# Optimization experiments

Hardware: AMD Instinct MI355X
Metric: run time of the kernel (lower is better)

The kernel has to match this reference:

```python
import jax, jax.numpy as jnp
import numpy as np

B, N, C, H = 16, 1024, 768, 12
HD = C // H               # head_dim = 64
SCALE = HD ** -0.5
EPS = 1e-5


def ter_quant(w):
    """BitNet-b1.58 ternary weight quantization with straight-through estimator.
    Per-tensor scale = mean(|W|); weights rounded to {-1,0,1}*scale."""
    s = jnp.mean(jnp.abs(w))
    wq = jnp.round(jnp.clip(w / (s + EPS), -1.0, 1.0)) * s
    return w + jax.lax.stop_gradient(wq - w)


def setup_inputs() -> dict:
    key = jax.random.key(0)
    k1, k2, k3 = jax.random.split(key, 3)
    return {
        "x": jax.random.normal(k1, (B, N, C), dtype=jnp.float32),
        "w_qkv": jax.random.normal(k2, (3 * C, C), dtype=jnp.float32) * 0.02,
        "w_proj": jax.random.normal(k3, (C, C), dtype=jnp.float32) * 0.02,
        "b_proj": jnp.zeros((C,), dtype=jnp.float32),
    }


def reference(x, w_qkv, w_proj, b_proj):
    # ternary-quantized QKV projection: [B,N,C] @ [C,3C] -> [B,N,3C]
    qkv = jnp.einsum('bnc,dc->bnd', x, ter_quant(w_qkv))
    qkv = qkv.reshape(B, N, 3, H, HD).transpose(2, 0, 3, 1, 4)  # [3,B,H,N,HD]
    q, k, v = qkv[0], qkv[1], qkv[2]
    # manual softmax attention (dropout p=0 -> identity)
    attn = jax.nn.softmax(jnp.einsum('bhqd,bhkd->bhqk', q, k) * SCALE, axis=-1)
    out = jnp.einsum('bhqk,bhkd->bhqd', attn, v)          # [B,H,N,HD]
    out = out.transpose(0, 2, 1, 3).reshape(B, N, C)      # [B,N,C]
    # ternary-quantized output projection
    return jnp.einsum('bnc,dc->bnd', out, ter_quant(w_proj)) + b_proj
```

## Files before the change

### kernel.cpp

```cpp
#include <hip/hip_runtime.h>
#include <hip/hip_bf16.h>

#define DEVI __device__ __forceinline__

typedef __bf16 bf16_t;
typedef __bf16 bf16x8 __attribute__((ext_vector_type(8)));
typedef float  f32x4  __attribute__((ext_vector_type(4)));
typedef float  f32x16 __attribute__((ext_vector_type(16)));
typedef unsigned short u16x4 __attribute__((ext_vector_type(4)));
typedef unsigned int   u32x4 __attribute__((ext_vector_type(4)));

typedef __attribute__((address_space(1))) unsigned int gas_u32;
typedef __attribute__((address_space(3))) unsigned int las_u32;

#define LOG2E 1.4426950408889634f

DEVI void gload16(const void* g, void* l) {
  __builtin_amdgcn_global_load_lds((gas_u32*)g, (las_u32*)l, 16, 0, 0);
}

DEVI unsigned short bf16bits(float f) {
  bf16_t b = (bf16_t)f;
  return __builtin_bit_cast(unsigned short, b);
}

DEVI unsigned pk2(float a, float b) {
  return ((unsigned)bf16bits(b) << 16) | (unsigned)bf16bits(a);
}

DEVI unsigned short quant1(float wv, double s) {
  double tq = (double)wv / s;
  tq = fmin(fmax(tq, -1.0), 1.0);
  return __builtin_bit_cast(unsigned short, (bf16_t)(float)rint(tq));
}

__global__ __launch_bounds__(256) void k_abssum2(const float* __restrict__ wq,
                                                 const float* __restrict__ wp,
                                                 double* __restrict__ partials) {
  __shared__ double sm[256];
  const int t = threadIdx.x, bid = blockIdx.x;
  const float* __restrict__ w = (bid < 256) ? wq : wp;
  const int n = (bid < 256) ? 1769472 : 589824;
  const int b0 = bid & 255;
  double acc = 0.0;
  for (int i = b0 * 256 + t; i < n; i += 65536)
    acc += (double)fabsf(w[i]);
  sm[t] = acc;
  __syncthreads();
  #pragma unroll
  for (int s = 128; s > 0; s >>= 1) {
    if (t < s) sm[t] += sm[t + s];
    __syncthreads();
  }
  if (t == 0) partials[bid] = sm[0];
}

__global__ __launch_bounds__(256) void k_reduce2(const double* __restrict__ partials,
                                                 double* __restrict__ outs) {
  __shared__ double sm[256];
  const int t = threadIdx.x;
  sm[t] = partials[blockIdx.x * 256 + t];
  __syncthreads();
  #pragma unroll
  for (int s = 128; s > 0; s >>= 1) {
    if (t < s) sm[t] += sm[t + s];
    __syncthreads();
  }
  if (t == 0) outs[blockIdx.x] = sm[0];
}

__global__ __launch_bounds__(256) void k_prep(
    const float* __restrict__ wq, const float* __restrict__ wp,
    const float* __restrict__ x, const double* __restrict__ scl,
    bf16_t* __restrict__ wqs, bf16_t* __restrict__ wps, bf16_t* __restrict__ xbf) {
  const int bid = blockIdx.x, t = threadIdx.x;
  if (bid < 1728) {
    const double s = scl[0] * (1.0 / 1769472.0) + 1e-5;
    const int i = bid * 256 + t;
    const float4 v = ((const float4*)wq)[i];
    u16x4 o = { quant1(v.x, s), quant1(v.y, s), quant1(v.z, s), quant1(v.w, s) };
    ((u16x4*)wqs)[i] = o;
  } else if (bid < 2304) {
    const double s = scl[1] * (1.0 / 589824.0) + 1e-5;
    const int i = (bid - 1728) * 256 + t;
    const float4 v = ((const float4*)wp)[i];
    u16x4 o = { quant1(v.x, s), quant1(v.y, s), quant1(v.z, s), quant1(v.w, s) };
    ((u16x4*)wps)[i] = o;
  } else {
    const int i = (bid - 2304) * 256 + t;
    const float4 v = ((const float4*)x)[i];
    u16x4 pk = { bf16bits(v.x), bf16bits(v.y), bf16bits(v.z), bf16bits(v.w) };
    ((u16x4*)xbf)[i] = pk;
  }
}

template<int MODE>
__global__ __launch_bounds__(512, 2) void k_gemm(
    const bf16_t* __restrict__ A, const bf16_t* __restrict__ Bw,
    const double* __restrict__ sumptr, double invn,
    bf16_t* __restrict__ Qb, bf16_t* __restrict__ Kb, bf16_t* __restrict__ VTb,
    const float* __restrict__ bias, float* __restrict__ Out,
    int nxblk)
{
  __shared__ __align__(16) char lds[147456];
  const int t = threadIdx.x, l = t & 63, w = t >> 6;

  const int nblk = nxblk * 64;
  const int flat = blockIdx.y * nxblk + blockIdx.x;
  const int per = nblk >> 3;
  const int swz = (flat & 7) * per + (flat >> 3);
  const int m0 = (swz / nxblk) * 256, n0 = (swz % nxblk) * 128;

  const int wm = w >> 1, wn = w & 1;
  const int srow = l >> 3, scol = (l & 7) * 8;
  const int lq = l & 15, lh = l >> 4;
  const int gcol = scol ^ (srow * 8);

  auto sA = [&](int slot, int kts, int ha, int c) {
    const int row = ha * 128 + (c * 8 + w) * 8 + srow;
    gload16(A + (size_t)(m0 + row) * 768 + kts * 64 + gcol,
            lds + slot * 49152 + ha * 16384 + (c * 8 + w) * 1024);
  };
  auto sB = [&](int slot, int kts, int c) {
    const int row = (c * 8 + w) * 8 + srow;
    gload16(Bw + (size_t)(n0 + row) * 768 + kts * 64 + gcol,
            lds + slot * 49152 + 32768 + (c * 8 + w) * 1024);
  };

  f32x4 acc[4][4] = {};

  sA(0, 0, 0, 0); sA(0, 0, 0, 1); sA(0, 0, 1, 0); sA(0, 0, 1, 1);
  sB(0, 0, 0);    sB(0, 0, 1);
  sA(1, 1, 0, 0); sA(1, 1, 0, 1); sA(1, 1, 1, 0); sA(1, 1, 1, 1);
  sB(1, 1, 0);    sB(1, 1, 1);
  asm volatile("s_waitcnt vmcnt(6)" ::: "memory");
  asm volatile("s_barrier" ::: "memory");

  #pragma unroll
  for (int kt = 0; kt < 12; ++kt) {
    const char* cA = lds + (kt % 3) * 49152;
    const char* cB = cA + 32768;
    const int st3 = (kt + 2) % 3;
    const bool stg = (kt < 10);

    {
      bf16x8 af[4], bf[4];
      #pragma unroll
      for (int i = 0; i < 4; ++i) {
        const int row = wm * 64 + i * 16 + lq;
        af[i] = *(const bf16x8*)(cA + row * 128 + ((lh * 16) ^ ((row & 7) << 4)));
      }
      #pragma unroll
      for (int j = 0; j < 4; ++j) {
        const int row = wn * 64 + j * 16 + lq;
        bf[j] = *(const bf16x8*)(cB + row * 128 + ((lh * 16) ^ ((row & 7) << 4)));
      }
      if (stg) { sA(st3, kt + 2, 0, 0); sA(st3, kt + 2, 0, 1); sB(st3, kt + 2, 0); }
      asm volatile("s_barrier" ::: "memory");
      __builtin_amdgcn_s_setprio(1);
      #pragma unroll
      for (int i = 0; i < 4; ++i)
        #pragma unroll
        for (int j = 0; j < 4; ++j)
          acc[i][j] = __builtin_amdgcn_mfma_f32_16x16x32_bf16(af[i], bf[j], acc[i][j], 0, 0, 0);
      __builtin_amdgcn_s_setprio(0);
      asm volatile("s_barrier" ::: "memory");
    }
    {
      bf16x8 af[4], bf[4];
      #pragma unroll
      for (int i = 0; i < 4; ++i) {
        const int row = wm * 64 + i * 16 + lq;
        af[i] = *(const bf16x8*)(cA + row * 128 + ((64 + lh * 16) ^ ((row & 7) << 4)));
      }
      #pragma unroll
      for (int j = 0; j < 4; ++j) {
        const int row = wn * 64 + j * 16 + lq;
        bf[j] = *(const bf16x8*)(cB + row * 128 + ((64 + lh * 16) ^ ((row & 7) << 4)));
      }
      if (stg) { sA(st3, kt + 2, 1, 0); sA(st3, kt + 2, 1, 1); sB(st3, kt + 2, 1); }
      asm volatile("s_barrier" ::: "memory");
      __builtin_amdgcn_s_setprio(1);
      #pragma unroll
      for (int i = 0; i < 4; ++i)
        #pragma unroll
        for (int j = 0; j < 4; ++j)
          acc[i][j] = __builtin_amdgcn_mfma_f32_16x16x32_bf16(af[i], bf[j], acc[i][j], 0, 0, 0);
      __builtin_amdgcn_s_setprio(0);
      if (stg) asm volatile("s_waitcnt vmcnt(6)" ::: "memory");
      else     asm volatile("s_waitcnt vmcnt(0)" ::: "memory");
      asm volatile("s_barrier" ::: "memory");
    }
  }

  const float s = (float)((*sumptr) * invn);
  char* st = lds + w * 8192;

  const int mrow0 = m0 + wm * 64;
  const int b = mrow0 >> 10, nbase = mrow0 & 1023;

  if (MODE == 0) {
    const int d0 = n0 + wn * 64;
    const int which = d0 / 768;
    const int hh = (d0 >> 6) % 12;
    if (which == 2) {
      #pragma unroll
      for (int j = 0; j < 4; ++j)
        #pragma unroll
        for (int i = 0; i < 4; ++i)
          #pragma unroll
          for (int r = 0; r < 4; ++r) {
            const int rowd = j * 16 + lq;
            const int coln = (i * 16 + lh * 4 + r) * 2;
            *(bf16_t*)(st + rowd * 128 + (coln ^ ((rowd & 7) << 4))) =
                (bf16_t)(acc[i][j][r] * s);
          }
    } else {
      const float sc = (which == 0) ? s * 0.125f * LOG2E : s;
      #pragma unroll
      for (int i = 0; i < 4; ++i)
        #pragma unroll
        for (int j = 0; j < 4; ++j)
          #pragma unroll
          for (int r = 0; r < 4; ++r) {
            const int row = i * 16 + lh * 4 + r;
            const int colb = (j * 16 + lq) * 2;
            *(bf16_t*)(st + row * 128 + (colb ^ ((row & 7) << 4))) =
                (bf16_t)(acc[i][j][r] * sc);
          }
    }
    __syncthreads();
    if (which == 0) {
      char* dstp = (char*)(Qb + ((size_t)(b * 12 + hh) * 1024 + nbase) * 64);
      #pragma unroll
      for (int it = 0; it < 8; ++it) {
        const int row = it * 8 + (l >> 3);
        const int colb = (l & 7) * 16;
        const u32x4 v = *(const u32x4*)(st + row * 128 + (colb ^ ((row & 7) << 4)));
        *(u32x4*)(dstp + row * 128 + colb) = v;
      }
    } else {
      bf16_t* base = (which == 1) ? Kb : VTb;
      char* dstp = (char*)base + ((((size_t)(b * 12 + hh)) * 16 + (nbase >> 6)) << 13);
      #pragma unroll
      for (int j = 0; j < 8; ++j) {
        const int row = (j >> 2) * 32 + (l & 31);
        const int colb = (j & 3) * 32 + (l >> 5) * 16;
        const u32x4 v = *(const u32x4*)(st + row * 128 + (colb ^ ((row & 7) << 4)));
        *(u32x4*)(dstp + j * 1024 + l * 16) = v;
      }
    }
  } else {
    const int d0 = n0 + wn * 64;
    const float4 bv = *(const float4*)(bias + d0 + (l & 15) * 4);
    #pragma unroll
    for (int c = 0; c < 2; ++c) {
      #pragma unroll
      for (int i2 = 0; i2 < 2; ++i2) {
        const int i = c * 2 + i2;
        #pragma unroll
        for (int j = 0; j < 4; ++j)
          #pragma unroll
          for (int r = 0; r < 4; ++r) {
            const int row = i2 * 16 + lh * 4 + r;
            const int colb = (j * 16 + lq) * 4;
            *(float*)(st + row * 256 + (colb ^ ((row & 7) << 4))) = acc[i][j][r] * s;
          }
      }
      __syncthreads();
      #pragma unroll
      for (int it = 0; it < 8; ++it) {
        const int row = it * 4 + (l >> 4);
        const int colb = (l & 15) * 16;
        float4 v = *(const float4*)(st + row * 256 + (colb ^ ((row & 7) << 4)));
        v.x += bv.x; v.y += bv.y; v.z += bv.z; v.w += bv.w;
        *(float4*)((char*)(Out + (size_t)(mrow0 + c * 32 + row) * 768 + d0) + colb) = v;
      }
      __syncthreads();
    }
  }
}

__global__ __launch_bounds__(256, 4) void k_attn(
    const bf16_t* __restrict__ Qb, const bf16_t* __restrict__ Kb,
    const bf16_t* __restrict__ VTb, bf16_t* __restrict__ Ob)
{
  __shared__ bf16_t smem[2][2][4096];
  const int t = threadIdx.x, l = t & 63, w = t >> 6;
  const int bh = blockIdx.x, qb = blockIdx.y;
  const int lq = l & 31, hi = l >> 5;
  const int q0 = qb * 128 + w * 32;

  const char* Kg = (const char*)(Kb + (size_t)bh * 65536);
  const char* Vg = (const char*)(VTb + (size_t)bh * 65536);

  bf16x8 qf[4];
  #pragma unroll
  for (int ks = 0; ks < 4; ++ks)
    qf[ks] = *(const bf16x8*)(Qb + (size_t)bh * 65536 + (q0 + lq) * 64 + ks * 16 + hi * 8);

  f32x16 ot0 = {}, ot1 = {};
  float mrun = -1e30f, lrun = 0.0f;

  auto stage = [&](int buf, int kt) {
    #pragma unroll
    for (int i = 0; i < 2; ++i) {
      const int c = i * 4 + w;
      gload16(Kg + (size_t)kt * 8192 + c * 1024 + l * 16, &smem[buf][0][c * 512]);
      gload16(Vg + (size_t)kt * 8192 + c * 1024 + l * 16, &smem[buf][1][c * 512]);
    }
  };

  stage(0, 0);
  __syncthreads();

  for (int kt = 0; kt < 16; ++kt) {
    const int cur = kt & 1;
    if (kt < 15) stage(cur ^ 1, kt + 1);
    const char* lK = (const char*)smem[cur][0];
    const char* lV = (const char*)smem[cur][1];
    const int lo = l * 16;

    f32x16 st0 = {}, st1 = {};
    __builtin_amdgcn_s_setprio(1);
    #pragma unroll
    for (int ks = 0; ks < 4; ++ks) {
      const bf16x8 k0 = *(const bf16x8*)(lK + ks * 1024 + lo);
      const bf16x8 k1 = *(const bf16x8*)(lK + (4 + ks) * 1024 + lo);
      st0 = __builtin_amdgcn_mfma_f32_32x32x16_bf16(k0, qf[ks], st0, 0, 0, 0);
      st1 = __builtin_amdgcn_mfma_f32_32x32x16_bf16(k1, qf[ks], st1, 0, 0, 0);
    }
    __builtin_amdgcn_s_setprio(0);

    float m8[8];
    #pragma unroll
    for (int r = 0; r < 8; ++r)
      m8[r] = fmaxf(fmaxf(st0[r], st0[r + 8]), fmaxf(st1[r], st1[r + 8]));
    float pmax = fmaxf(fmaxf(fmaxf(m8[0], m8[1]), fmaxf(m8[2], m8[3])),
                       fmaxf(fmaxf(m8[4], m8[5]), fmaxf(m8[6], m8[7])));
    pmax = fmaxf(pmax, __shfl_xor(pmax, 32));

    if (__any(pmax > mrun + 8.0f)) {
      const float mn = fmaxf(mrun, pmax);
      const float corr = __builtin_amdgcn_exp2f(mrun - mn);
      lrun *= corr;
      #pragma unroll
      for (int r = 0; r < 16; ++r) { ot0[r] *= corr; ot1[r] *= corr; }
      mrun = mn;
    }

    float psum = 0.0f;
    __builtin_amdgcn_s_setprio(1);
    auto grp = [&](const f32x16& stv, int r0, int g) {
      float p[8];
      #pragma unroll
      for (int e = 0; e < 8; ++e) p[e] = __builtin_amdgcn_exp2f(stv[r0 + e] - mrun);
      psum += ((p[0] + p[1]) + (p[2] + p[3])) + ((p[4] + p[5]) + (p[6] + p[7]));
      const unsigned w0 = pk2(p[0], p[1]), w1 = pk2(p[2], p[3]);
      const unsigned w2 = pk2(p[4], p[5]), w3 = pk2(p[6], p[7]);
      const unsigned x0 = __shfl_xor(w0, 32), x1 = __shfl_xor(w1, 32);
      const unsigned x2 = __shfl_xor(w2, 32), x3 = __shfl_xor(w3, 32);
      const u32x4 fw = hi ? u32x4{x2, x3, w2, w3} : u32x4{w0, w1, x0, x1};
      const bf16x8 pf = __builtin_bit_cast(bf16x8, fw);
      const bf16x8 v0 = *(const bf16x8*)(lV + g * 1024 + lo);
      const bf16x8 v1 = *(const bf16x8*)(lV + (4 + g) * 1024 + lo);
      ot0 = __builtin_amdgcn_mfma_f32_32x32x16_bf16(v0, pf, ot0, 0, 0, 0);
      ot1 = __builtin_amdgcn_mfma_f32_32x32x16_bf16(v1, pf, ot1, 0, 0, 0);
    };
    grp(st0, 0, 0);
    grp(st0, 8, 1);
    grp(st1, 0, 2);
    grp(st1, 8, 3);
    __builtin_amdgcn_s_setprio(0);
    psum += __shfl_xor(psum, 32);
    lrun += psum;

    __syncthreads();
  }

  __syncthreads();
  bf16_t* olds = (bf16_t*)smem + w * 2048;
  const float inv = 1.0f / lrun;
  #pragma unroll
  for (int dt = 0; dt < 2; ++dt)
    #pragma unroll
    for (int rg = 0; rg < 4; ++rg) {
      u16x4 pk;
      #pragma unroll
      for (int e = 0; e < 4; ++e)
        pk[e] = bf16bits((dt ? ot1[rg * 4 + e] : ot0[rg * 4 + e]) * inv);
      const int d = rg * 8 + hi * 4 + dt * 32;
      *(u16x4*)((char*)olds + ((lq * 128 + d * 2) ^ ((lq & 7) << 4))) = pk;
    }
  __syncthreads();
  const int b = bh / 12, h = bh % 12;
  #pragma unroll
  for (int i = 0; i < 8; ++i) {
    const int q = i * 4 + (l >> 4);
    const u16x4 v =
        *(const u16x4*)((const char*)olds + ((q * 128 + (l & 15) * 8) ^ ((q & 7) << 4)));
    *(u16x4*)(Ob + ((size_t)(b * 1024 + q0 + q)) * 768 + h * 64 + (l & 15) * 4) = v;
  }
}

extern "C" void kernel_launch(void* const* d_in, const int* in_sizes, int n_in,
                              void* d_out, int out_size, void* d_ws, size_t ws_size,
                              hipStream_t stream) {
  const float* x      = (const float*)d_in[0];
  const float* w_qkv  = (const float*)d_in[1];
  const float* w_proj = (const float*)d_in[2];
  const float* b_proj = (const float*)d_in[3];
  float* out = (float*)d_out;

  char* ws = (char*)d_ws;
  double* part  = (double*)ws;
  double* scl   = (double*)(ws + 4096);
  bf16_t* xbf   = (bf16_t*)(ws + 4608);
  bf16_t* wqs   = (bf16_t*)(ws + 4608 + 25165824);
  bf16_t* wps   = (bf16_t*)(ws + 4608 + 25165824 + 3538944);
  bf16_t* qbuf  = (bf16_t*)(ws + 4608 + 25165824 + 3538944 + 1179648);
  bf16_t* kbuf  = qbuf + 12582912;
  bf16_t* vtbuf = kbuf + 12582912;
  bf16_t* aout  = xbf;

  k_abssum2<<<512, 256, 0, stream>>>(w_qkv, w_proj, part);
  k_reduce2<<<2, 256, 0, stream>>>(part, scl);
  k_prep<<<14592, 256, 0, stream>>>(w_qkv, w_proj, x, scl, wqs, wps, xbf);
  k_gemm<0><<<dim3(18, 64), 512, 0, stream>>>(xbf, wqs, scl, 1.0 / 1769472.0,
                                              qbuf, kbuf, vtbuf, nullptr, nullptr, 18);
  k_attn<<<dim3(192, 8), 256, 0, stream>>>(qbuf, kbuf, vtbuf, aout);
  k_gemm<1><<<dim3(6, 64), 512, 0, stream>>>(aout, wps, scl + 1, 1.0 / 589824.0,
                                             nullptr, nullptr, nullptr, b_proj, out, 6);
}
```

Baseline: 203.4 us.

## Halve GEMM K-tile to 32, drop LDS swizzle and raise occupancy target

Restructures the bf16 GEMM main loop to use 32-wide K tiles instead of 64. This halves the triple-buffered LDS footprint and cuts staging to three 16-byte global-to-LDS loads per thread per tile. The XOR swizzle on LDS reads is removed, and there is now a single barrier per K-step instead of two. The launch bound is raised to request 4 blocks per CU to improve latency hiding. The risks are LDS bank conflicts from the unswizzled 64-byte row stride, and heavy register pressure or spills: the tighter bound caps VGPRs while the loop still holds 64 accumulators, and LDS capacity may still allow only two blocks per CU.

```diff
diff --git a/kernel.cpp b/kernel.cpp
--- a/kernel.cpp
+++ b/kernel.cpp
@@ -95,14 +95,14 @@
 }
 
 template<int MODE>
-__global__ __launch_bounds__(512, 2) void k_gemm(
+__global__ __launch_bounds__(512, 4) void k_gemm(
     const bf16_t* __restrict__ A, const bf16_t* __restrict__ Bw,
     const double* __restrict__ sumptr, double invn,
     bf16_t* __restrict__ Qb, bf16_t* __restrict__ Kb, bf16_t* __restrict__ VTb,
     const float* __restrict__ bias, float* __restrict__ Out,
     int nxblk)
 {
-  __shared__ __align__(16) char lds[147456];
+  __shared__ __align__(16) char lds[73728];
   const int t = threadIdx.x, l = t & 63, w = t >> 6;
 
   const int nblk = nxblk * 64;
@@ -112,85 +112,50 @@
   const int m0 = (swz / nxblk) * 256, n0 = (swz % nxblk) * 128;
 
   const int wm = w >> 1, wn = w & 1;
-  const int srow = l >> 3, scol = (l & 7) * 8;
   const int lq = l & 15, lh = l >> 4;
-  const int gcol = scol ^ (srow * 8);
-
-  auto sA = [&](int slot, int kts, int ha, int c) {
-    const int row = ha * 128 + (c * 8 + w) * 8 + srow;
-    gload16(A + (size_t)(m0 + row) * 768 + kts * 64 + gcol,
-            lds + slot * 49152 + ha * 16384 + (c * 8 + w) * 1024);
+  const int grow = t >> 2, gs8 = (t & 3) * 8;
+
+  auto stage = [&](int slot, int kts) {
+    char* dst = lds + slot * 24576;
+    gload16(A + (size_t)(m0 + grow) * 768 + kts * 32 + gs8, dst + t * 16);
+    gload16(A + (size_t)(m0 + 128 + grow) * 768 + kts * 32 + gs8, dst + 8192 + t * 16);
+    gload16(Bw + (size_t)(n0 + grow) * 768 + kts * 32 + gs8, dst + 16384 + t * 16);
   };
-  auto sB = [&](int slot, int kts, int c) {
-    const int row = (c * 8 + w) * 8 + srow;
-    gload16(Bw + (size_t)(n0 + row) * 768 + kts * 64 + gcol,
-            lds + slot * 49152 + 32768 + (c * 8 + w) * 1024);
-  };
 
   f32x4 acc[4][4] = {};
 
-  sA(0, 0, 0, 0); sA(0, 0, 0, 1); sA(0, 0, 1, 0); sA(0, 0, 1, 1);
-  sB(0, 0, 0);    sB(0, 0, 1);
-  sA(1, 1, 0, 0); sA(1, 1, 0, 1); sA(1, 1, 1, 0); sA(1, 1, 1, 1);
-  sB(1, 1, 0);    sB(1, 1, 1);
-  asm volatile("s_waitcnt vmcnt(6)" ::: "memory");
+  stage(0, 0);
+  stage(1, 1);
+  asm volatile("s_waitcnt vmcnt(3)" ::: "memory");
   asm volatile("s_barrier" ::: "memory");
 
   #pragma unroll
-  for (int kt = 0; kt < 12; ++kt) {
-    const char* cA = lds + (kt % 3) * 49152;
-    const char* cB = cA + 32768;
-    const int st3 = (kt + 2) % 3;
-    const bool stg = (kt < 10);
-
-    {
-      bf16x8 af[4], bf[4];
-      #pragma unroll
-      for (int i = 0; i < 4; ++i) {
-        const int row = wm * 64 + i * 16 + lq;
-        af[i] = *(const bf16x8*)(cA + row * 128 + ((lh * 16) ^ ((row & 7) << 4)));
-      }
-      #pragma unroll
-      for (int j = 0; j < 4; ++j) {
-        const int row = wn * 64 + j * 16 + lq;
-        bf[j] = *(const bf16x8*)(cB + row * 128 + ((lh * 16) ^ ((row & 7) << 4)));
-      }
-      if (stg) { sA(st3, kt + 2, 0, 0); sA(st3, kt + 2, 0, 1); sB(st3, kt + 2, 0); }
-      asm volatile("s_barrier" ::: "memory");
-      __builtin_amdgcn_s_setprio(1);
-      #pragma unroll
-      for (int i = 0; i < 4; ++i)
-        #pragma unroll
-        for (int j = 0; j < 4; ++j)
-          acc[i][j] = __builtin_amdgcn_mfma_f32_16x16x32_bf16(af[i], bf[j], acc[i][j], 0, 0, 0);
-      __builtin_amdgcn_s_setprio(0);
-      asm volatile("s_barrier" ::: "memory");
-    }
-    {
-      bf16x8 af[4], bf[4];
-      #pragma unroll
-      for (int i = 0; i < 4; ++i) {
-        const int row = wm * 64 + i * 16 + lq;
-        af[i] = *(const bf16x8*)(cA + row * 128 + ((64 + lh * 16) ^ ((row & 7) << 4)));
-      }
-      #pragma unroll
-      for (int j = 0; j < 4; ++j) {
-        const int row = wn * 64 + j * 16 + lq;
-        bf[j] = *(const bf16x8*)(cB + row * 128 + ((64 + lh * 16) ^ ((row & 7) << 4)));
-      }
-      if (stg) { sA(st3, kt + 2, 1, 0); sA(st3, kt + 2, 1, 1); sB(st3, kt + 2, 1); }
-      asm volatile("s_barrier" ::: "memory");
-      __builtin_amdgcn_s_setprio(1);
-      #pragma unroll
-      for (int i = 0; i < 4; ++i)
-        #pragma unroll
-        for (int j = 0; j < 4; ++j)
-          acc[i][j] = __builtin_amdgcn_mfma_f32_16x16x32_bf16(af[i], bf[j], acc[i][j], 0, 0, 0);
-      __builtin_amdgcn_s_setprio(0);
-      if (stg) asm volatile("s_waitcnt vmcnt(6)" ::: "memory");
-      else     asm volatile("s_waitcnt vmcnt(0)" ::: "memory");
-      asm volatile("s_barrier" ::: "memory");
-    }
+  for (int kt = 0; kt < 24; ++kt) {
+    const char* cA = lds + (kt % 3) * 24576 + (wm >> 1) * 8192;
+    const char* cB = lds + (kt % 3) * 24576 + 16384;
+
+    bf16x8 af[4], bf[4];
+    #pragma unroll
+    for (int i = 0; i < 4; ++i) {
+      const int lrow = (wm & 1) * 64 + i * 16 + lq;
+      af[i] = *(const bf16x8*)(cA + lrow * 64 + lh * 16);
+    }
+    #pragma unroll
+    for (int j = 0; j < 4; ++j) {
+      const int row = wn * 64 + j * 16 + lq;
+      bf[j] = *(const bf16x8*)(cB + row * 64 + lh * 16);
+    }
+    if (kt < 22) stage((kt + 2) % 3, kt + 2);
+    __builtin_amdgcn_s_setprio(1);
+    #pragma unroll
+    for (int i = 0; i < 4; ++i)
+      #pragma unroll
+      for (int j = 0; j < 4; ++j)
+        acc[i][j] = __builtin_amdgcn_mfma_f32_16x16x32_bf16(af[i], bf[j], acc[i][j], 0, 0, 0);
+    __builtin_amdgcn_s_setprio(0);
+    if (kt <= 21)      asm volatile("s_waitcnt vmcnt(3)" ::: "memory");
+    else if (kt == 22) asm volatile("s_waitcnt vmcnt(0)" ::: "memory");
+    asm volatile("s_barrier" ::: "memory");
   }
 
   const float s = (float)((*sumptr) * invn);
```

After: 196.1 us. 1.04x faster.
